# Kernel optimization log

Measured on AMD Instinct MI355X. Metric: run time of the kernel, lower is better.

## Reference

```python
import jax, jax.numpy as jnp
import numpy as np

K_NEIGHBORS = 32  # nsample

def setup_inputs() -> dict:
    key = jax.random.key(0)
    ks = jax.random.split(key, 16)
    B, C, N = 4, 3, 4096
    def w(k, shape):
        return jax.random.normal(k, shape, dtype=jnp.float32) * 0.05
    inp = {"x": jax.random.normal(ks[0], (B, C, N), dtype=jnp.float32)}
    # three scale MLPs share shapes -> stack along leading scale axis (s=3)
    inp["sW0"] = w(ks[1], (3, 64, 3));    inp["sb0"] = w(ks[2], (3, 64))
    inp["sW1"] = w(ks[3], (3, 64, 64));   inp["sb1"] = w(ks[4], (3, 64))
    inp["sW2"] = w(ks[5], (3, 128, 64));  inp["sb2"] = w(ks[6], (3, 128))
    inp["gW0"] = w(ks[7], (256, 384));    inp["gb0"] = w(ks[8], (256,))
    inp["gW1"] = w(ks[9], (1024, 256));   inp["gb1"] = w(ks[10], (1024,))
    inp["mW0"] = w(ks[11], (256, 1024));  inp["mb0"] = w(ks[12], (256,))
    inp["mW1"] = w(ks[13], (128, 256));   inp["mb1"] = w(ks[14], (128,))
    return inp

def _knn_idx(x, k):
    # x: [B, 3, N] channels-first points; k nearest neighbors excluding self
    pts = jnp.swapaxes(x, 1, 2)                       # [B, N, 3]
    sq = jnp.sum(pts * pts, axis=-1)                  # [B, N]
    d = sq[:, :, None] + sq[:, None, :] - 2.0 * jnp.einsum('bnc,bmc->bnm', pts, pts)
    _, idx = jax.lax.top_k(-d, k + 1)                 # nearest first (self at 0)
    return idx[:, :, 1:]                              # [B, N, k]

def reference(x, sW0, sb0, sW1, sb1, sW2, sb2, gW0, gb0, gW1, gb1, mW0, mb0, mW1, mb1):
    B, C, N = x.shape
    # radius is unused by sample_and_group_knn -> all three scales share knn idx
    idx = _knn_idx(x, K_NEIGHBORS)                    # [B, N, K]
    # gather: per-batch x[:, idx[b]] -> [B, C, N, K]
    g = jax.vmap(lambda xf, i: xf[:, i])(x, idx)
    # three shared-weight 1x1-conv MLPs, batched over scale axis s
    h = jax.nn.relu(jnp.einsum('bcnk,soc->sbonk', g, sW0) + sb0[:, None, :, None, None])
    h = jax.nn.relu(jnp.einsum('sbcnk,soc->sbonk', h, sW1) + sb1[:, None, :, None, None])
    h = jax.nn.relu(jnp.einsum('sbcnk,soc->sbonk', h, sW2) + sb2[:, None, :, None, None])
    p = jnp.max(h, axis=-1)                           # [3, B, 128, N] max over neighbors
    point = jnp.moveaxis(p, 0, 1).reshape(B, 3 * p.shape[2], N)  # concat scales -> [B, 384, N]
    gf = jax.nn.relu(jnp.einsum('bcn,oc->bon', point, gW0) + gb0[None, :, None])
    gf = jax.nn.relu(jnp.einsum('bcn,oc->bon', gf, gW1) + gb1[None, :, None])     # [B,1024,N]
    msf = jax.nn.relu(jnp.einsum('bcn,oc->bon', gf, mW0) + mb0[None, :, None])
    msf = jax.nn.relu(jnp.einsum('bcn,oc->bon', msf, mW1) + mb1[None, :, None])   # [B,128,N]
    global_feature = jnp.max(gf, axis=-1)             # [B, 1024]
    return (global_feature, msf)
```

## Files before the change

### kernel.cpp

```cpp
#include <hip/hip_runtime.h>
#include <hip/hip_bf16.h>

#define NPTS 4096
#define KNN  32

typedef __attribute__((ext_vector_type(8))) short short8;
typedef __attribute__((ext_vector_type(4))) float floatx4;
typedef unsigned short u16x2 __attribute__((ext_vector_type(2)));

__device__ __forceinline__ unsigned short f2bf(float f) {
    unsigned u = __float_as_uint(f);
    u = (u + 0x7FFFu + ((u >> 16) & 1u)) >> 16;
    return (unsigned short)u;
}

__global__ __launch_bounds__(256) void prep_all(
    const float* __restrict__ x, float4* __restrict__ pts4,
    const float* __restrict__ gW0, const float* __restrict__ gW1,
    const float* __restrict__ mW0, const float* __restrict__ mW1,
    const float* __restrict__ sW1, const float* __restrict__ sW2,
    unsigned short* __restrict__ Wb0, unsigned short* __restrict__ Wb1,
    unsigned short* __restrict__ Wb2, unsigned short* __restrict__ Wb3,
    unsigned short* __restrict__ Wb4, unsigned short* __restrict__ Wb5)
{
    const int blk = blockIdx.x, t = threadIdx.x;
    if (blk < 64) {
        const int i = blk * 256 + t;
        const int b = i >> 12, n = i & (NPTS - 1);
        const float* xb = x + (size_t)b * 3 * NPTS;
        const float qx = xb[n], qy = xb[NPTS + n], qz = xb[2 * NPTS + n];
        pts4[i] = make_float4(qx, qy, qz, qx * qx + qy * qy + qz * qz);
    } else {
        const int wi = (blk - 64) * 256 + t;
        float v; unsigned short* dst;
        if (wi < 98304)       { v = gW0[wi];          dst = Wb0 + wi; }
        else if (wi < 360448) { v = gW1[wi - 98304];  dst = Wb1 + (wi - 98304); }
        else if (wi < 622592) { v = mW0[wi - 360448]; dst = Wb2 + (wi - 360448); }
        else if (wi < 655360) { v = mW1[wi - 622592]; dst = Wb3 + (wi - 622592); }
        else if (wi < 667648) { v = sW1[wi - 655360]; dst = Wb4 + (wi - 655360); }
        else                  { v = sW2[wi - 667648]; dst = Wb5 + (wi - 667648); }
        *dst = f2bf(v);
    }
}

__global__ __launch_bounds__(256) void knn_kernel16(const float4* __restrict__ pts4,
                                                    int* __restrict__ knn_out)
{
    __shared__ unsigned sred[2][4];
    __shared__ unsigned minS[256];
    __shared__ unsigned long long C[256];
    __shared__ unsigned ccnt;

    const int t = threadIdx.x, wid = t >> 6, lane = t & 63;
    const int q = blockIdx.x, b = q >> 12, n = q & (NPTS - 1);
    const float4* P = pts4 + ((size_t)b << 12);
    const float4 s = P[n];
    const float px = s.x, py = s.y, pz = s.z, sqn = s.w;

    if (t == 0) ccnt = 0u;

    unsigned key[16];
    #pragma unroll
    for (int g = 0; g < 4; ++g) {
        float4 c0 = P[((g * 4 + 0) << 8) + t];
        float4 c1 = P[((g * 4 + 1) << 8) + t];
        float4 c2 = P[((g * 4 + 2) << 8) + t];
        float4 c3 = P[((g * 4 + 3) << 8) + t];
        float d0 = (sqn + c0.w) - 2.0f * (px * c0.x + py * c0.y + pz * c0.z);
        float d1 = (sqn + c1.w) - 2.0f * (px * c1.x + py * c1.y + pz * c1.z);
        float d2 = (sqn + c2.w) - 2.0f * (px * c2.x + py * c2.y + pz * c2.z);
        float d3 = (sqn + c3.w) - 2.0f * (px * c3.x + py * c3.y + pz * c3.z);
        unsigned u0 = __float_as_uint(d0), u1 = __float_as_uint(d1);
        unsigned u2 = __float_as_uint(d2), u3 = __float_as_uint(d3);
        key[g * 4 + 0] = (u0 & 0x80000000u) ? ~u0 : (u0 | 0x80000000u);
        key[g * 4 + 1] = (u1 & 0x80000000u) ? ~u1 : (u1 | 0x80000000u);
        key[g * 4 + 2] = (u2 & 0x80000000u) ? ~u2 : (u2 | 0x80000000u);
        key[g * 4 + 3] = (u3 & 0x80000000u) ? ~u3 : (u3 | 0x80000000u);
    }

    unsigned tm = key[0];
    #pragma unroll
    for (int r = 1; r < 16; ++r) tm = (key[r] < tm) ? key[r] : tm;
    minS[t] = tm;
    __syncthreads();

    unsigned m0 = minS[lane];
    unsigned m1 = minS[lane + 64];
    unsigned m2 = minS[lane + 128];
    unsigned m3 = minS[lane + 192];
    m0 = (m1 < m0) ? m1 : m0;
    m2 = (m3 < m2) ? m3 : m2;
    m0 = (m2 < m0) ? m2 : m0;

    unsigned lo = 0u, hi = 0xFFFFFFFFu;
    for (int i = 0; i < 32; ++i) {
        const unsigned mid = lo + ((hi - lo) >> 1);
        const unsigned cnt = (unsigned)__popcll(__ballot(m0 <= mid));
        if (cnt >= 33u) hi = mid; else lo = mid + 1u;
    }
    const unsigned thr0 = hi;

    #pragma unroll
    for (int r = 0; r < 16; ++r) {
        if (key[r] <= thr0) {
            unsigned p = atomicAdd(&ccnt, 1u);
            if (p < 256u)
                C[p] = ((unsigned long long)key[r] << 32) |
                       (unsigned)((r << 8) + t);
        }
    }
    __syncthreads();

    int nc = (int)ccnt;
    if (nc > 256) {
        if (t == 0) ccnt = 0u;
        int pp = 0;
        auto countLE = [&](unsigned thr) -> unsigned {
            unsigned c = 0;
            #pragma unroll
            for (int r = 0; r < 16; ++r)
                c += (unsigned)__popcll(__ballot(key[r] <= thr));
            if (lane == 0) sred[pp & 1][wid] = c;
            __syncthreads();
            const unsigned g = sred[pp & 1][0] + sred[pp & 1][1] +
                               sred[pp & 1][2] + sred[pp & 1][3];
            ++pp;
            return g;
        };
        unsigned lo2 = 0x100u, hi2 = 0x1FEu, cntHi = 4096u;
        for (int it = 0; it < 8; ++it) {
            const unsigned mid = (lo2 + hi2) >> 1;
            const unsigned g = countLE((mid << 23) | 0x7FFFFFu);
            if (g >= 33u) { hi2 = mid; cntHi = g; } else lo2 = mid + 1u;
        }
        unsigned loK = lo2 << 23;
        unsigned hiK = (lo2 << 23) | 0x7FFFFFu;
        unsigned cntF = cntHi;
        while (cntF > 256u && loK < hiK) {
            const unsigned midK = loK + ((hiK - loK) >> 1);
            const unsigned c = countLE(midK);
            if (c >= 33u) { hiK = midK; cntF = c; } else loK = midK + 1u;
        }
        const unsigned thrF = hiK;
        #pragma unroll
        for (int r = 0; r < 16; ++r) {
            if (key[r] <= thrF) {
                unsigned p = atomicAdd(&ccnt, 1u);
                if (p < 256u)
                    C[p] = ((unsigned long long)key[r] << 32) |
                           (unsigned)((r << 8) + t);
            }
        }
        __syncthreads();
        nc = (int)ccnt; if (nc > 256) nc = 256;
    }

    if (t < nc) {
        const unsigned long long me = C[t];
        int rank = 0;
        for (int j = 0; j < nc; ++j) rank += (C[j] < me) ? 1 : 0;
        if (rank >= 1 && rank <= KNN)
            knn_out[(size_t)q * KNN + (rank - 1)] = (int)(me & 0xFFFFFFFFu);
    }
}

__global__ __launch_bounds__(256) void pointmlp_mfma(
    const float* __restrict__ x,
    const float* __restrict__ sW0, const float* __restrict__ sb0,
    const unsigned short* __restrict__ W1b, const float* __restrict__ sb1,
    const unsigned short* __restrict__ W2b, const float* __restrict__ sb2,
    unsigned short* __restrict__ F)
{
    __shared__ __align__(16) unsigned short W1s[64 * 72];
    __shared__ __align__(16) unsigned short W2s[128 * 72];
    __shared__ __align__(16) unsigned short h0T[32 * 72];
    __shared__ __align__(16) unsigned short h1T[32 * 72];
    __shared__ float W0s[192];
    __shared__ float b0s[64], b1s[64], b2s[128];
    __shared__ float pts[3 * 33];

    const int t = threadIdx.x;
    const int s = blockIdx.y;
    const int tile = blockIdx.x;
    const int b = tile >> 7;
    const int j0 = (tile & 127) << 5;
    const float* xb = x + (size_t)b * 3 * NPTS;

    if (t < 192) W0s[t] = sW0[s * 192 + t];
    if (t < 64) b0s[t] = sb0[s * 64 + t];
    if (t >= 64 && t < 128) b1s[t - 64] = sb1[s * 64 + (t - 64)];
    if (t < 128) b2s[t] = sb2[s * 128 + t];
    if (t < 96) { int c = t >> 5, p = t & 31; pts[c * 33 + p] = xb[c * NPTS + j0 + p]; }
    {
        const int o = t & 63, qq = t >> 6;
        const unsigned short* src = W1b + (size_t)s * 4096 + o * 64 + qq * 16;
        *(uint4*)&W1s[o * 72 + qq * 16]     = *(const uint4*)src;
        *(uint4*)&W1s[o * 72 + qq * 16 + 8] = *(const uint4*)(src + 8);
    }
    {
        const int o2 = t & 127, hh = t >> 7;
        const unsigned short* src = W2b + (size_t)s * 8192 + o2 * 64 + hh * 32;
        *(uint4*)&W2s[o2 * 72 + hh * 32]      = *(const uint4*)src;
        *(uint4*)&W2s[o2 * 72 + hh * 32 + 8]  = *(const uint4*)(src + 8);
        *(uint4*)&W2s[o2 * 72 + hh * 32 + 16] = *(const uint4*)(src + 16);
        *(uint4*)&W2s[o2 * 72 + hh * 32 + 24] = *(const uint4*)(src + 24);
    }
    __syncthreads();

    {
        const int p = t & 31, og = t >> 5;
        const float xx = pts[p], yy = pts[33 + p], zz = pts[66 + p];
        unsigned short hv[8];
        #pragma unroll
        for (int r = 0; r < 8; ++r) {
            const int o = og * 8 + r;
            float a = b0s[o] + W0s[o * 3] * xx + W0s[o * 3 + 1] * yy
                    + W0s[o * 3 + 2] * zz;
            hv[r] = f2bf(fmaxf(a, 0.0f));
        }
        *(uint4*)&h0T[p * 72 + og * 8] = *(const uint4*)hv;
    }
    __syncthreads();

    const int w = t >> 6, lane = t & 63, quad = lane >> 4, l15 = lane & 15;

    {
        #pragma unroll
        for (int ni = 0; ni < 2; ++ni) {
            floatx4 acc = (floatx4){0.f, 0.f, 0.f, 0.f};
            #pragma unroll
            for (int k0 = 0; k0 < 2; ++k0) {
                short8 aF = *(const short8*)&W1s[(w * 16 + l15) * 72 + k0 * 32 + quad * 8];
                short8 bF = *(const short8*)&h0T[(ni * 16 + l15) * 72 + k0 * 32 + quad * 8];
                acc = __builtin_amdgcn_mfma_f32_16x16x32_bf16(aF, bF, acc, 0, 0, 0);
            }
            const int m0 = w * 16 + quad * 4;
            const int p = ni * 16 + l15;
            ushort4 pk;
            pk.x = f2bf(fmaxf(acc[0] + b1s[m0 + 0], 0.f));
            pk.y = f2bf(fmaxf(acc[1] + b1s[m0 + 1], 0.f));
            pk.z = f2bf(fmaxf(acc[2] + b1s[m0 + 2], 0.f));
            pk.w = f2bf(fmaxf(acc[3] + b1s[m0 + 3], 0.f));
            *(ushort4*)&h1T[p * 72 + m0] = pk;
        }
    }
    __syncthreads();

    {
        #pragma unroll
        for (int mi = 0; mi < 2; ++mi) {
            const int m0 = (w * 2 + mi) * 16;
            #pragma unroll
            for (int ni = 0; ni < 2; ++ni) {
                floatx4 acc = (floatx4){0.f, 0.f, 0.f, 0.f};
                #pragma unroll
                for (int k0 = 0; k0 < 2; ++k0) {
                    short8 aF = *(const short8*)&W2s[(m0 + l15) * 72 + k0 * 32 + quad * 8];
                    short8 bF = *(const short8*)&h1T[(ni * 16 + l15) * 72 + k0 * 32 + quad * 8];
                    acc = __builtin_amdgcn_mfma_f32_16x16x32_bf16(aF, bF, acc, 0, 0, 0);
                }
                const int o2 = m0 + quad * 4;
                const int j = j0 + ni * 16 + l15;
                ushort4 pk;
                pk.x = f2bf(fmaxf(acc[0] + b2s[o2 + 0], 0.f));
                pk.y = f2bf(fmaxf(acc[1] + b2s[o2 + 1], 0.f));
                pk.z = f2bf(fmaxf(acc[2] + b2s[o2 + 2], 0.f));
                pk.w = f2bf(fmaxf(acc[3] + b2s[o2 + 3], 0.f));
                *(ushort4*)&F[((size_t)b * NPTS + j) * 384 + s * 128 + o2] = pk;
            }
        }
    }
}

__global__ __launch_bounds__(192) void maxgather_bf16(
    const unsigned short* __restrict__ F, const int* __restrict__ knn,
    unsigned short* __restrict__ pt)
{
    __shared__ int idxS[KNN];
    const int q = blockIdx.x;
    const int b = q >> 12;
    const int t = threadIdx.x;
    if (t < KNN) idxS[t] = knn[(size_t)q * KNN + t];
    __syncthreads();
    const unsigned short* Fb = F + (size_t)b * NPTS * 384 + t * 2;
    u16x2 m = (u16x2)0;
    #pragma unroll 8
    for (int k = 0; k < KNN; ++k) {
        u16x2 v = *(const u16x2*)(Fb + (size_t)idxS[k] * 384);
        m = __builtin_elementwise_max(m, v);
    }
    *(u16x2*)(pt + (size_t)q * 384 + t * 2) = m;
}

template<int DO_ROWMAX>
__global__ __launch_bounds__(256) void gemm_bf16(
    const unsigned short* __restrict__ Wb, const unsigned short* __restrict__ Bt,
    const float* __restrict__ bias, void* __restrict__ outp,
    float* __restrict__ gfeat, int M, int K)
{
    __shared__ __align__(16) unsigned short As[128 * 40];
    __shared__ __align__(16) unsigned short Bs[128 * 40];
    __shared__ float biasS[128];
    __shared__ int redI[128];

    const int t = threadIdx.x;
    const int b = blockIdx.z;
    const int m0 = blockIdx.x * 128;
    const int n0 = blockIdx.y * 128;
    if (t < 128) biasS[t] = bias[m0 + t];
    if (DO_ROWMAX && t < 128) redI[t] = 0;

    const int wave = t >> 6, lane = t & 63, quad = lane >> 4, l15 = lane & 15;
    const int wr = wave >> 1, wc = wave & 1;

    const int am = t & 127, akh = t >> 7;
    const unsigned short* Wp = Wb + (size_t)(m0 + am) * K + akh * 16;
    const int bn = t >> 2, bq = t & 3;
    const unsigned short* Bp = Bt + ((size_t)b * NPTS + n0) * K;

    floatx4 acc[16];
    #pragma unroll
    for (int i = 0; i < 16; ++i) acc[i] = (floatx4){0.f, 0.f, 0.f, 0.f};

    const int nk = K >> 5;
    for (int kt = 0; kt < nk; ++kt) {
        const int k0 = kt << 5;
        uint4 av0 = *(const uint4*)(Wp + k0);
        uint4 av1 = *(const uint4*)(Wp + k0 + 8);
        uint4 bv0 = *(const uint4*)(Bp + (size_t)bn * K + k0 + bq * 8);
        uint4 bv1 = *(const uint4*)(Bp + (size_t)(bn + 64) * K + k0 + bq * 8);
        __syncthreads();
        {
            uint4* dst = (uint4*)&As[am * 40 + akh * 16];
            dst[0] = av0;
            dst[1] = av1;
            *(uint4*)&Bs[bn * 40 + bq * 8] = bv0;
            *(uint4*)&Bs[(bn + 64) * 40 + bq * 8] = bv1;
        }
        __syncthreads();
        short8 af[4], bfv[4];
        #pragma unroll
        for (int i = 0; i < 4; ++i)
            af[i] = *(const short8*)&As[(wr * 64 + i * 16 + l15) * 40 + quad * 8];
        #pragma unroll
        for (int j = 0; j < 4; ++j)
            bfv[j] = *(const short8*)&Bs[(wc * 64 + j * 16 + l15) * 40 + quad * 8];
        #pragma unroll
        for (int i = 0; i < 4; ++i)
            #pragma unroll
            for (int j = 0; j < 4; ++j)
                acc[i * 4 + j] = __builtin_amdgcn_mfma_f32_16x16x32_bf16(
                    af[i], bfv[j], acc[i * 4 + j], 0, 0, 0);
    }

    #pragma unroll
    for (int i = 0; i < 4; ++i) {
        const int mbase = wr * 64 + i * 16 + quad * 4;
        float rm0 = 0.f, rm1 = 0.f, rm2 = 0.f, rm3 = 0.f;
        #pragma unroll
        for (int j = 0; j < 4; ++j) {
            const int n = n0 + wc * 64 + j * 16 + l15;
            float v0 = fmaxf(acc[i * 4 + j][0] + biasS[mbase + 0], 0.f);
            float v1 = fmaxf(acc[i * 4 + j][1] + biasS[mbase + 1], 0.f);
            float v2 = fmaxf(acc[i * 4 + j][2] + biasS[mbase + 2], 0.f);
            float v3 = fmaxf(acc[i * 4 + j][3] + biasS[mbase + 3], 0.f);
            if (DO_ROWMAX) {
                rm0 = fmaxf(rm0, v0); rm1 = fmaxf(rm1, v1);
                rm2 = fmaxf(rm2, v2); rm3 = fmaxf(rm3, v3);
            }
            ushort4 pk;
            pk.x = f2bf(v0); pk.y = f2bf(v1); pk.z = f2bf(v2); pk.w = f2bf(v3);
            *(ushort4*)((unsigned short*)outp +
                        ((size_t)b * NPTS + n) * M + m0 + mbase) = pk;
        }
        if (DO_ROWMAX) {
            atomicMax(&redI[mbase + 0], __float_as_int(rm0));
            atomicMax(&redI[mbase + 1], __float_as_int(rm1));
            atomicMax(&redI[mbase + 2], __float_as_int(rm2));
            atomicMax(&redI[mbase + 3], __float_as_int(rm3));
        }
    }
    if (DO_ROWMAX) {
        __syncthreads();
        if (t < 128)
            atomicMax((int*)&gfeat[(size_t)b * 1024 + m0 + t], redI[t]);
    }
}

__global__ __launch_bounds__(256) void fused_head(
    const unsigned short* __restrict__ Wb2, const unsigned short* __restrict__ Wb3,
    const float* __restrict__ mb0, const float* __restrict__ mb1,
    const unsigned short* __restrict__ gft, float* __restrict__ outp)
{
    __shared__ __align__(16) unsigned short As[256 * 40];
    __shared__ __align__(16) unsigned short Bs[64 * 40];
    __shared__ __align__(16) unsigned short H[64 * 264];
    __shared__ float b0s[256];
    __shared__ float b1s[128];

    const int t = threadIdx.x;
    const int n0 = blockIdx.x * 64;
    const int b = blockIdx.y;
    b0s[t] = mb0[t];
    if (t < 128) b1s[t] = mb1[t];

    const int wave = t >> 6, lane = t & 63, quad = lane >> 4, l15 = lane & 15;

    const unsigned short* Ap = Wb2 + (size_t)t * 1024;
    const int bn = t >> 2, bq = t & 3;
    const unsigned short* Bp = gft + ((size_t)b * NPTS + n0) * 1024;

    floatx4 acc[16];
    #pragma unroll
    for (int i = 0; i < 16; ++i) acc[i] = (floatx4){0.f, 0.f, 0.f, 0.f};

    for (int kt = 0; kt < 32; ++kt) {
        const int k0 = kt << 5;
        uint4 a0 = *(const uint4*)(Ap + k0);
        uint4 a1 = *(const uint4*)(Ap + k0 + 8);
        uint4 a2 = *(const uint4*)(Ap + k0 + 16);
        uint4 a3 = *(const uint4*)(Ap + k0 + 24);
        uint4 bv = *(const uint4*)(Bp + (size_t)bn * 1024 + k0 + bq * 8);
        __syncthreads();
        *(uint4*)&As[t * 40 + 0]  = a0;
        *(uint4*)&As[t * 40 + 8]  = a1;
        *(uint4*)&As[t * 40 + 16] = a2;
        *(uint4*)&As[t * 40 + 24] = a3;
        *(uint4*)&Bs[bn * 40 + bq * 8] = bv;
        __syncthreads();
        short8 af[4], bfv[4];
        #pragma unroll
        for (int i = 0; i < 4; ++i)
            af[i] = *(const short8*)&As[(wave * 64 + i * 16 + l15) * 40 + quad * 8];
        #pragma unroll
        for (int j = 0; j < 4; ++j)
            bfv[j] = *(const short8*)&Bs[(j * 16 + l15) * 40 + quad * 8];
        #pragma unroll
        for (int i = 0; i < 4; ++i)
            #pragma unroll
            for (int j = 0; j < 4; ++j)
                acc[i * 4 + j] = __builtin_amdgcn_mfma_f32_16x16x32_bf16(
                    af[i], bfv[j], acc[i * 4 + j], 0, 0, 0);
    }
    #pragma unroll
    for (int i = 0; i < 4; ++i) {
        const int mbase = wave * 64 + i * 16 + quad * 4;
        #pragma unroll
        for (int j = 0; j < 4; ++j) {
            const int nl = j * 16 + l15;
            ushort4 pk;
            pk.x = f2bf(fmaxf(acc[i * 4 + j][0] + b0s[mbase + 0], 0.f));
            pk.y = f2bf(fmaxf(acc[i * 4 + j][1] + b0s[mbase + 1], 0.f));
            pk.z = f2bf(fmaxf(acc[i * 4 + j][2] + b0s[mbase + 2], 0.f));
            pk.w = f2bf(fmaxf(acc[i * 4 + j][3] + b0s[mbase + 3], 0.f));
            *(ushort4*)&H[nl * 264 + mbase] = pk;
        }
    }

    floatx4 acc2[8];
    #pragma unroll
    for (int i = 0; i < 8; ++i) acc2[i] = (floatx4){0.f, 0.f, 0.f, 0.f};
    const int am2 = t & 127, ah = t >> 7;

    for (int kt = 0; kt < 8; ++kt) {
        const int k0 = kt << 5;
        uint4 a0 = *(const uint4*)(Wb3 + (size_t)am2 * 256 + k0 + ah * 16);
        uint4 a1 = *(const uint4*)(Wb3 + (size_t)am2 * 256 + k0 + ah * 16 + 8);
        __syncthreads();
        *(uint4*)&As[am2 * 40 + ah * 16]     = a0;
        *(uint4*)&As[am2 * 40 + ah * 16 + 8] = a1;
        __syncthreads();
        short8 af2[2], bf2[4];
        #pragma unroll
        for (int i = 0; i < 2; ++i)
            af2[i] = *(const short8*)&As[(wave * 32 + i * 16 + l15) * 40 + quad * 8];
        #pragma unroll
        for (int j = 0; j < 4; ++j)
            bf2[j] = *(const short8*)&H[(j * 16 + l15) * 264 + k0 + quad * 8];
        #pragma unroll
        for (int i = 0; i < 2; ++i)
            #pragma unroll
            for (int j = 0; j < 4; ++j)
                acc2[i * 4 + j] = __builtin_amdgcn_mfma_f32_16x16x32_bf16(
                    af2[i], bf2[j], acc2[i * 4 + j], 0, 0, 0);
    }
    #pragma unroll
    for (int i = 0; i < 2; ++i) {
        const int m2 = wave * 32 + i * 16 + quad * 4;
        #pragma unroll
        for (int j = 0; j < 4; ++j) {
            const int n = n0 + j * 16 + l15;
            float* o = outp + ((size_t)b * 128 + m2) * NPTS + n;
            o[0 * NPTS] = fmaxf(acc2[i * 4 + j][0] + b1s[m2 + 0], 0.f);
            o[1 * NPTS] = fmaxf(acc2[i * 4 + j][1] + b1s[m2 + 1], 0.f);
            o[2 * NPTS] = fmaxf(acc2[i * 4 + j][2] + b1s[m2 + 2], 0.f);
            o[3 * NPTS] = fmaxf(acc2[i * 4 + j][3] + b1s[m2 + 3], 0.f);
        }
    }
}

extern "C" void kernel_launch(void* const* d_in, const int* in_sizes, int n_in,
                              void* d_out, int out_size, void* d_ws, size_t ws_size,
                              hipStream_t stream)
{
    const float* x   = (const float*)d_in[0];
    const float* sW0 = (const float*)d_in[1];
    const float* sb0 = (const float*)d_in[2];
    const float* sW1 = (const float*)d_in[3];
    const float* sb1 = (const float*)d_in[4];
    const float* sW2 = (const float*)d_in[5];
    const float* sb2 = (const float*)d_in[6];
    const float* gW0 = (const float*)d_in[7];
    const float* gb0 = (const float*)d_in[8];
    const float* gW1 = (const float*)d_in[9];
    const float* gb1 = (const float*)d_in[10];
    const float* mW0 = (const float*)d_in[11];
    const float* mb0 = (const float*)d_in[12];
    const float* mW1 = (const float*)d_in[13];
    const float* mb1 = (const float*)d_in[14];
    float* outp = (float*)d_out;

    char* ws = (char*)d_ws;
    int*            idx     = (int*)(ws);
    float4*         pts4    = (float4*)(ws + 2097152u);
    unsigned short* Wb0     = (unsigned short*)(ws + 2359296u);
    unsigned short* Wb1     = (unsigned short*)(ws + 2555904u);
    unsigned short* Wb2     = (unsigned short*)(ws + 3080192u);
    unsigned short* Wb3     = (unsigned short*)(ws + 3604480u);
    unsigned short* Wb4     = (unsigned short*)(ws + 3670016u);
    unsigned short* Wb5     = (unsigned short*)(ws + 3694592u);
    unsigned short* F       = (unsigned short*)(ws + 4194304u);
    unsigned short* point_t = (unsigned short*)(ws + 18874368u);
    unsigned short* gf0t    = (unsigned short*)(ws + 33554432u);
    unsigned short* gft     = (unsigned short*)(ws + 50331648u);

    prep_all<<<dim3(2768), dim3(256), 0, stream>>>(
        x, pts4, gW0, gW1, mW0, mW1, sW1, sW2, Wb0, Wb1, Wb2, Wb3, Wb4, Wb5);
    knn_kernel16<<<dim3(16384), dim3(256), 0, stream>>>(pts4, idx);
    pointmlp_mfma<<<dim3(512, 3), dim3(256), 0, stream>>>(
        x, sW0, sb0, Wb4, sb1, Wb5, sb2, F);
    maxgather_bf16<<<dim3(16384), dim3(192), 0, stream>>>(F, idx, point_t);
    gemm_bf16<0><<<dim3(2, 32, 4), dim3(256), 0, stream>>>(
        Wb0, point_t, gb0, gf0t, nullptr, 256, 384);
    gemm_bf16<1><<<dim3(8, 32, 4), dim3(256), 0, stream>>>(
        Wb1, gf0t, gb1, gft, outp, 1024, 256);
    fused_head<<<dim3(64, 4), dim3(256), 0, stream>>>(
        Wb2, Wb3, mb0, mb1, gft, outp + 4096);
}
```

Measured before the change: 250.8 us.

## Shorten KNN threshold search, fixed-size rank pass, and halve fused_head tile width

The KNN kernel now bisects on the top 16 bits of the per-thread minima (16 iterations instead of 32), uses a branchless key flip, and when few candidates exist ranks them with a fully unrolled 64-wide loop over sentinel-padded shared memory. The fused_head kernel's point tile drops from 64 to 32 columns, doubling the grid to 128x4 blocks to raise occupancy and reduce LDS and registers per block. The coarser threshold may admit more candidates, making the overflow fallback more likely, and smaller head tiles reload the weight matrix twice as often.

Measured after the change: 244.1 us. 1.03x faster.

```diff
diff --git a/kernel.cpp b/kernel.cpp
--- a/kernel.cpp
+++ b/kernel.cpp
@@ -43,7 +43,7 @@
     }
 }
 
-__global__ __launch_bounds__(256) void knn_kernel16(const float4* __restrict__ pts4,
+__global__ __launch_bounds__(256) void knn_kernel17(const float4* __restrict__ pts4,
                                                     int* __restrict__ knn_out)
 {
     __shared__ unsigned sred[2][4];
@@ -58,6 +58,7 @@
     const float px = s.x, py = s.y, pz = s.z, sqn = s.w;
 
     if (t == 0) ccnt = 0u;
+    C[t] = 0xFFFFFFFFFFFFFFFFULL;
 
     unsigned key[16];
     #pragma unroll
@@ -72,10 +73,10 @@
         float d3 = (sqn + c3.w) - 2.0f * (px * c3.x + py * c3.y + pz * c3.z);
         unsigned u0 = __float_as_uint(d0), u1 = __float_as_uint(d1);
         unsigned u2 = __float_as_uint(d2), u3 = __float_as_uint(d3);
-        key[g * 4 + 0] = (u0 & 0x80000000u) ? ~u0 : (u0 | 0x80000000u);
-        key[g * 4 + 1] = (u1 & 0x80000000u) ? ~u1 : (u1 | 0x80000000u);
-        key[g * 4 + 2] = (u2 & 0x80000000u) ? ~u2 : (u2 | 0x80000000u);
-        key[g * 4 + 3] = (u3 & 0x80000000u) ? ~u3 : (u3 | 0x80000000u);
+        key[g * 4 + 0] = u0 ^ (((unsigned)((int)u0 >> 31)) | 0x80000000u);
+        key[g * 4 + 1] = u1 ^ (((unsigned)((int)u1 >> 31)) | 0x80000000u);
+        key[g * 4 + 2] = u2 ^ (((unsigned)((int)u2 >> 31)) | 0x80000000u);
+        key[g * 4 + 3] = u3 ^ (((unsigned)((int)u3 >> 31)) | 0x80000000u);
     }
 
     unsigned tm = key[0];
@@ -92,13 +93,14 @@
     m2 = (m3 < m2) ? m3 : m2;
     m0 = (m2 < m0) ? m2 : m0;
 
-    unsigned lo = 0u, hi = 0xFFFFFFFFu;
-    for (int i = 0; i < 32; ++i) {
-        const unsigned mid = lo + ((hi - lo) >> 1);
-        const unsigned cnt = (unsigned)__popcll(__ballot(m0 <= mid));
+    const unsigned ms16 = m0 >> 16;
+    unsigned lo = 0u, hi = 0xFFFFu;
+    for (int i = 0; i < 16; ++i) {
+        const unsigned mid = (lo + hi) >> 1;
+        const unsigned cnt = (unsigned)__popcll(__ballot(ms16 <= mid));
         if (cnt >= 33u) hi = mid; else lo = mid + 1u;
     }
-    const unsigned thr0 = hi;
+    const unsigned thr0 = (hi << 16) | 0xFFFFu;
 
     #pragma unroll
     for (int r = 0; r < 16; ++r) {
@@ -112,7 +114,9 @@
     __syncthreads();
 
     int nc = (int)ccnt;
+    bool fell_back = false;
     if (nc > 256) {
+        fell_back = true;
         if (t == 0) ccnt = 0u;
         int pp = 0;
         auto countLE = [&](unsigned thr) -> unsigned {
@@ -155,12 +159,23 @@
         nc = (int)ccnt; if (nc > 256) nc = 256;
     }
 
-    if (t < nc) {
-        const unsigned long long me = C[t];
-        int rank = 0;
-        for (int j = 0; j < nc; ++j) rank += (C[j] < me) ? 1 : 0;
-        if (rank >= 1 && rank <= KNN)
-            knn_out[(size_t)q * KNN + (rank - 1)] = (int)(me & 0xFFFFFFFFu);
+    if (!fell_back && nc <= 64) {
+        if (t < 64) {
+            const unsigned long long me = C[t];
+            int rank = 0;
+            #pragma unroll
+            for (int j = 0; j < 64; ++j) rank += (C[j] < me) ? 1 : 0;
+            if (rank >= 1 && rank <= KNN)
+                knn_out[(size_t)q * KNN + (rank - 1)] = (int)(me & 0xFFFFFFFFu);
+        }
+    } else {
+        if (t < nc) {
+            const unsigned long long me = C[t];
+            int rank = 0;
+            for (int j = 0; j < nc; ++j) rank += (C[j] < me) ? 1 : 0;
+            if (rank >= 1 && rank <= KNN)
+                knn_out[(size_t)q * KNN + (rank - 1)] = (int)(me & 0xFFFFFFFFu);
+        }
     }
 }
 
@@ -393,13 +408,13 @@
     const unsigned short* __restrict__ gft, float* __restrict__ outp)
 {
     __shared__ __align__(16) unsigned short As[256 * 40];
-    __shared__ __align__(16) unsigned short Bs[64 * 40];
-    __shared__ __align__(16) unsigned short H[64 * 264];
+    __shared__ __align__(16) unsigned short Bs[32 * 40];
+    __shared__ __align__(16) unsigned short H[32 * 264];
     __shared__ float b0s[256];
     __shared__ float b1s[128];
 
     const int t = threadIdx.x;
-    const int n0 = blockIdx.x * 64;
+    const int n0 = blockIdx.x * 32;
     const int b = blockIdx.y;
     b0s[t] = mb0[t];
     if (t < 128) b1s[t] = mb1[t];
@@ -410,9 +425,9 @@
     const int bn = t >> 2, bq = t & 3;
     const unsigned short* Bp = gft + ((size_t)b * NPTS + n0) * 1024;
 
-    floatx4 acc[16];
-    #pragma unroll
-    for (int i = 0; i < 16; ++i) acc[i] = (floatx4){0.f, 0.f, 0.f, 0.f};
+    floatx4 acc[8];
+    #pragma unroll
+    for (int i = 0; i < 8; ++i) acc[i] = (floatx4){0.f, 0.f, 0.f, 0.f};
 
     for (int kt = 0; kt < 32; ++kt) {
         const int k0 = kt << 5;
@@ -420,46 +435,47 @@
         uint4 a1 = *(const uint4*)(Ap + k0 + 8);
         uint4 a2 = *(const uint4*)(Ap + k0 + 16);
         uint4 a3 = *(const uint4*)(Ap + k0 + 24);
-        uint4 bv = *(const uint4*)(Bp + (size_t)bn * 1024 + k0 + bq * 8);
+        uint4 bv;
+        if (bn < 32) bv = *(const uint4*)(Bp + (size_t)bn * 1024 + k0 + bq * 8);
         __syncthreads();
         *(uint4*)&As[t * 40 + 0]  = a0;
         *(uint4*)&As[t * 40 + 8]  = a1;
         *(uint4*)&As[t * 40 + 16] = a2;
         *(uint4*)&As[t * 40 + 24] = a3;
-        *(uint4*)&Bs[bn * 40 + bq * 8] = bv;
-        __syncthreads();
-        short8 af[4], bfv[4];
+        if (bn < 32) *(uint4*)&Bs[bn * 40 + bq * 8] = bv;
+        __syncthreads();
+        short8 af[4], bfv[2];
         #pragma unroll
         for (int i = 0; i < 4; ++i)
             af[i] = *(const short8*)&As[(wave * 64 + i * 16 + l15) * 40 + quad * 8];
         #pragma unroll
-        for (int j = 0; j < 4; ++j)
+        for (int j = 0; j < 2; ++j)
             bfv[j] = *(const short8*)&Bs[(j * 16 + l15) * 40 + quad * 8];
         #pragma unroll
         for (int i = 0; i < 4; ++i)
             #pragma unroll
-            for (int j = 0; j < 4; ++j)
-                acc[i * 4 + j] = __builtin_amdgcn_mfma_f32_16x16x32_bf16(
-                    af[i], bfv[j], acc[i * 4 + j], 0, 0, 0);
+            for (int j = 0; j < 2; ++j)
+                acc[i * 2 + j] = __builtin_amdgcn_mfma_f32_16x16x32_bf16(
+                    af[i], bfv[j], acc[i * 2 + j], 0, 0, 0);
     }
     #pragma unroll
     for (int i = 0; i < 4; ++i) {
         const int mbase = wave * 64 + i * 16 + quad * 4;
         #pragma unroll
-        for (int j = 0; j < 4; ++j) {
+        for (int j = 0; j < 2; ++j) {
             const int nl = j * 16 + l15;
             ushort4 pk;
-            pk.x = f2bf(fmaxf(acc[i * 4 + j][0] + b0s[mbase + 0], 0.f));
-            pk.y = f2bf(fmaxf(acc[i * 4 + j][1] + b0s[mbase + 1], 0.f));
-            pk.z = f2bf(fmaxf(acc[i * 4 + j][2] + b0s[mbase + 2], 0.f));
-            pk.w = f2bf(fmaxf(acc[i * 4 + j][3] + b0s[mbase + 3], 0.f));
+            pk.x = f2bf(fmaxf(acc[i * 2 + j][0] + b0s[mbase + 0], 0.f));
+            pk.y = f2bf(fmaxf(acc[i * 2 + j][1] + b0s[mbase + 1], 0.f));
+            pk.z = f2bf(fmaxf(acc[i * 2 + j][2] + b0s[mbase + 2], 0.f));
+            pk.w = f2bf(fmaxf(acc[i * 2 + j][3] + b0s[mbase + 3], 0.f));
             *(ushort4*)&H[nl * 264 + mbase] = pk;
         }
     }
 
-    floatx4 acc2[8];
-    #pragma unroll
-    for (int i = 0; i < 8; ++i) acc2[i] = (floatx4){0.f, 0.f, 0.f, 0.f};
+    floatx4 acc2[4];
+    #pragma unroll
+    for (int i = 0; i < 4; ++i) acc2[i] = (floatx4){0.f, 0.f, 0.f, 0.f};
     const int am2 = t & 127, ah = t >> 7;
 
     for (int kt = 0; kt < 8; ++kt) {
@@ -470,31 +486,31 @@
         *(uint4*)&As[am2 * 40 + ah * 16]     = a0;
         *(uint4*)&As[am2 * 40 + ah * 16 + 8] = a1;
         __syncthreads();
-        short8 af2[2], bf2[4];
+        short8 af2[2], bf2[2];
         #pragma unroll
         for (int i = 0; i < 2; ++i)
             af2[i] = *(const short8*)&As[(wave * 32 + i * 16 + l15) * 40 + quad * 8];
         #pragma unroll
-        for (int j = 0; j < 4; ++j)
+        for (int j = 0; j < 2; ++j)
             bf2[j] = *(const short8*)&H[(j * 16 + l15) * 264 + k0 + quad * 8];
         #pragma unroll
         for (int i = 0; i < 2; ++i)
             #pragma unroll
-            for (int j = 0; j < 4; ++j)
-                acc2[i * 4 + j] = __builtin_amdgcn_mfma_f32_16x16x32_bf16(
-                    af2[i], bf2[j], acc2[i * 4 + j], 0, 0, 0);
+            for (int j = 0; j < 2; ++j)
+                acc2[i * 2 + j] = __builtin_amdgcn_mfma_f32_16x16x32_bf16(
+                    af2[i], bf2[j], acc2[i * 2 + j], 0, 0, 0);
     }
     #pragma unroll
     for (int i = 0; i < 2; ++i) {
         const int m2 = wave * 32 + i * 16 + quad * 4;
         #pragma unroll
-        for (int j = 0; j < 4; ++j) {
+        for (int j = 0; j < 2; ++j) {
             const int n = n0 + j * 16 + l15;
             float* o = outp + ((size_t)b * 128 + m2) * NPTS + n;
-            o[0 * NPTS] = fmaxf(acc2[i * 4 + j][0] + b1s[m2 + 0], 0.f);
-            o[1 * NPTS] = fmaxf(acc2[i * 4 + j][1] + b1s[m2 + 1], 0.f);
-            o[2 * NPTS] = fmaxf(acc2[i * 4 + j][2] + b1s[m2 + 2], 0.f);
-            o[3 * NPTS] = fmaxf(acc2[i * 4 + j][3] + b1s[m2 + 3], 0.f);
+            o[0 * NPTS] = fmaxf(acc2[i * 2 + j][0] + b1s[m2 + 0], 0.f);
+            o[1 * NPTS] = fmaxf(acc2[i * 2 + j][1] + b1s[m2 + 1], 0.f);
+            o[2 * NPTS] = fmaxf(acc2[i * 2 + j][2] + b1s[m2 + 2], 0.f);
+            o[3 * NPTS] = fmaxf(acc2[i * 2 + j][3] + b1s[m2 + 3], 0.f);
         }
     }
 }
@@ -536,7 +552,7 @@
 
     prep_all<<<dim3(2768), dim3(256), 0, stream>>>(
         x, pts4, gW0, gW1, mW0, mW1, sW1, sW2, Wb0, Wb1, Wb2, Wb3, Wb4, Wb5);
-    knn_kernel16<<<dim3(16384), dim3(256), 0, stream>>>(pts4, idx);
+    knn_kernel17<<<dim3(16384), dim3(256), 0, stream>>>(pts4, idx);
     pointmlp_mfma<<<dim3(512, 3), dim3(256), 0, stream>>>(
         x, sW0, sb0, Wb4, sb1, Wb5, sb2, F);
     maxgather_bf16<<<dim3(16384), dim3(192), 0, stream>>>(F, idx, point_t);
@@ -544,6 +560,6 @@
         Wb0, point_t, gb0, gf0t, nullptr, 256, 384);
     gemm_bf16<1><<<dim3(8, 32, 4), dim3(256), 0, stream>>>(
         Wb1, gf0t, gb1, gft, outp, 1024, 256);
-    fused_head<<<dim3(64, 4), dim3(256), 0, stream>>>(
+    fused_head<<<dim3(128, 4), dim3(256), 0, stream>>>(
         Wb2, Wb3, mb0, mb1, gft, outp + 4096);
 }
```
